# Kernel optimization log

Measured on AMD Instinct MI355X. Metric: run time of the kernel, lower is better.

Reference implementation:

```python
import math
import jax, jax.numpy as jnp
import numpy as np

B, L, D, H = 2, 2048, 1024, 16
HD = D // H  # head_size = 64


def setup_inputs() -> dict:
    key = jax.random.key(0)
    kx, kk, kq, kv, ko = jax.random.split(key, 5)
    scale = 1.0 / math.sqrt(D)
    return {
        "x": jax.random.normal(kx, (B, L, D), dtype=jnp.float32),
        "Wk": jax.random.normal(kk, (D, D), dtype=jnp.float32) * scale,
        "Wq": jax.random.normal(kq, (D, D), dtype=jnp.float32) * scale,
        "Wv": jax.random.normal(kv, (D, D), dtype=jnp.float32) * scale,
        "Wo": jax.random.normal(ko, (D, D), dtype=jnp.float32) * scale,
    }


def reference(x, Wk, Wq, Wv, Wo):
    # Projections (torch Linear without bias; weights pre-stored as [in, out])
    k = (x @ Wk).reshape(B, L, H, HD)
    q = (x @ Wq).reshape(B, L, H, HD)
    v = (x @ Wv).reshape(B, L, H, HD)
    # Per-head causal attention, vectorized over heads instead of python loop
    inv_sqrt_hd = 1.0 / math.sqrt(HD)
    scores = jnp.einsum("blhd,bmhd->bhlm", q, k) * inv_sqrt_hd  # [B,H,L,L]
    causal = jnp.tril(jnp.ones((L, L), dtype=bool))
    scores = jnp.where(causal, scores, -jnp.inf)
    probs = jax.nn.softmax(scores, axis=-1)
    # Dropout is identity in eval mode (reference baseline is deterministic)
    out = jnp.einsum("bhlm,bmhd->blhd", probs, v).reshape(B, L, D)
    return out @ Wo
```

## Files before the change

### kernel.cpp

```cpp
#include <hip/hip_runtime.h>
#include <cstdint>

#define B_ 2
#define L_ 2048
#define D_ 1024
#define H_ 16
#define HD_ 64
#define ML_ (B_ * L_)
#define S_ (3 * D_)
#define QK_LD 2048

typedef __bf16 bf16;
typedef __attribute__((ext_vector_type(4))) __bf16 bf16x4;
typedef __attribute__((ext_vector_type(8))) __bf16 bf16x8;
typedef __attribute__((ext_vector_type(4))) float f32x4;
typedef __attribute__((ext_vector_type(16))) float f32x16;

__device__ __forceinline__ f32x4 mfma_16x16x32(bf16x8 a, bf16x8 b, f32x4 c) {
    return __builtin_amdgcn_mfma_f32_16x16x32_bf16(a, b, c, 0, 0, 0);
}
__device__ __forceinline__ f32x16 mfma_32x32x16(bf16x8 a, bf16x8 b, f32x16 c) {
    return __builtin_amdgcn_mfma_f32_32x32x16_bf16(a, b, c, 0, 0, 0);
}

#define GLDS16(g, l)                                                              \
    __builtin_amdgcn_global_load_lds((const __attribute__((address_space(1))) void*)(g), \
                                     (__attribute__((address_space(3))) void*)(l), 16, 0, 0)

__global__ __launch_bounds__(256) void cast_x_kernel(const float* __restrict__ in,
                                                     bf16* __restrict__ out, int n4) {
    int i = blockIdx.x * blockDim.x + threadIdx.x;
    if (i >= n4) return;
    float4 v = reinterpret_cast<const float4*>(in)[i];
    bf16x4 o;
    o[0] = (bf16)v.x; o[1] = (bf16)v.y; o[2] = (bf16)v.z; o[3] = (bf16)v.w;
    reinterpret_cast<bf16x4*>(out)[i] = o;
}

__global__ __launch_bounds__(1024) void transpose_w_kernel(const float* __restrict__ W,
                                                           bf16* __restrict__ Wt) {
    __shared__ float tile[32][33];
    int n0 = blockIdx.x * 32, k0 = blockIdx.y * 32;
    int tx = threadIdx.x, ty = threadIdx.y;
    tile[ty][tx] = W[(size_t)(k0 + ty) * D_ + n0 + tx];
    __syncthreads();
    Wt[(size_t)(n0 + ty) * D_ + k0 + tx] = (bf16)tile[tx][ty];
}

template <typename OutT>
__global__ __launch_bounds__(256) void gemm128_kernel(const bf16* __restrict__ A,
                                                      const bf16* __restrict__ Bt,
                                                      OutT* __restrict__ C,
                                                      bf16* __restrict__ vt,
                                                      int M, int N, int K, int ldc) {
    __shared__ bf16 As[128][32];
    __shared__ bf16 Bs[128][32];
    const int nwg = gridDim.x;
    const int bid = (blockIdx.x & 7) * (nwg >> 3) + (blockIdx.x >> 3);
    const int nb = N >> 7;
    const int bm = bid / nb, bn = bid % nb;
    const int m0 = bm << 7, n0 = bn << 7;
    const int t = threadIdx.x;
    const int lane = t & 63;
    const int w = t >> 6;
    const int wm = w >> 1, wn = w & 1;
    const int fr = lane & 15, fk = (lane >> 4) << 3;
    const int srow = (w << 5) + (lane >> 2);
    const int scol = (lane & 3) << 3;

    f32x4 acc[4][4] = {};
    for (int k0 = 0; k0 < K; k0 += 32) {
        const bf16* ga0 = &A[(size_t)(m0 + srow) * K + k0 + scol];
        const bf16* ga1 = &A[(size_t)(m0 + srow + 16) * K + k0 + scol];
        const bf16* gb0 = &Bt[(size_t)(n0 + srow) * K + k0 + scol];
        const bf16* gb1 = &Bt[(size_t)(n0 + srow + 16) * K + k0 + scol];
        __syncthreads();
        GLDS16(ga0, &As[(w << 5)][0]);
        GLDS16(ga1, &As[(w << 5) + 16][0]);
        GLDS16(gb0, &Bs[(w << 5)][0]);
        GLDS16(gb1, &Bs[(w << 5) + 16][0]);
        __syncthreads();
        bf16x8 a[4], b[4];
#pragma unroll
        for (int mt = 0; mt < 4; ++mt)
            a[mt] = *reinterpret_cast<const bf16x8*>(&As[(wm << 6) + (mt << 4) + fr][fk]);
#pragma unroll
        for (int nt = 0; nt < 4; ++nt)
            b[nt] = *reinterpret_cast<const bf16x8*>(&Bs[(wn << 6) + (nt << 4) + fr][fk]);
#pragma unroll
        for (int mt = 0; mt < 4; ++mt)
#pragma unroll
            for (int nt = 0; nt < 4; ++nt)
                acc[mt][nt] = mfma_16x16x32(a[mt], b[nt], acc[mt][nt]);
    }
    const int col = lane & 15, rq = (lane >> 4) << 2;
    if (vt != nullptr && n0 >= 2048) {
#pragma unroll
        for (int mt = 0; mt < 4; ++mt)
#pragma unroll
            for (int nt = 0; nt < 4; ++nt) {
                int cc = n0 - 2048 + (wn << 6) + (nt << 4) + col;
                int rrb = m0 + (wm << 6) + (mt << 4) + rq;
                int bb = rrb >> 11, l = rrb & (L_ - 1);
                size_t vrow = ((size_t)bb * H_ + (cc >> 6)) * HD_ + (cc & 63);
                bf16x4 pk;
#pragma unroll
                for (int reg = 0; reg < 4; ++reg) pk[reg] = (bf16)acc[mt][nt][reg];
                *reinterpret_cast<bf16x4*>(&vt[vrow * L_ + l]) = pk;
            }
    } else {
#pragma unroll
        for (int mt = 0; mt < 4; ++mt)
#pragma unroll
            for (int nt = 0; nt < 4; ++nt)
#pragma unroll
                for (int reg = 0; reg < 4; ++reg) {
                    int rr = m0 + (wm << 6) + (mt << 4) + rq + reg;
                    int cc = n0 + (wn << 6) + (nt << 4) + col;
                    C[(size_t)rr * ldc + cc] = (OutT)acc[mt][nt][reg];
                }
    }
}

__global__ __launch_bounds__(256) void attn_kernel(const bf16* __restrict__ qk,
                                                   const bf16* __restrict__ vt,
                                                   bf16* __restrict__ O) {
    __shared__ bf16 Olds[4][32][72];
    const int nbh = B_ * H_;
    const int qt = (L_ / 128) - 1 - (int)(blockIdx.x / nbh);
    const int bh = blockIdx.x % nbh;
    const int h = bh % H_, b = bh / H_;
    const int t = threadIdx.x, lane = t & 63, w = t >> 6;
    const int li = lane & 31, hi = lane >> 5;
    const int qg0 = qt * 128 + w * 32;
    const int q_g = qg0 + li;

    const bf16* kbase = qk + (size_t)b * L_ * QK_LD + D_ + h * HD_;
    const bf16* vbase = vt + (size_t)bh * HD_ * L_;

    const bf16* qrow_p = qk + (size_t)(b * L_ + q_g) * QK_LD + h * HD_ + hi * 8;
    bf16x8 qB[4];
#pragma unroll
    for (int c = 0; c < 4; ++c) qB[c] = *reinterpret_cast<const bf16x8*>(qrow_p + c * 16);

    f32x16 ot0 = {}, ot1 = {};
    float mrun = -1e30f, lsum = 0.f;
    const float c1 = 0.18033688011112042f;

    const int nkb = (qg0 + 31) / 64 + 1;
    for (int kb = 0; kb < nkb; ++kb) {
        const int c0 = kb * 64;
        f32x16 st0 = {}, st1 = {};
        const bf16* kp0 = kbase + (size_t)(c0 + li) * QK_LD + hi * 8;
        const bf16* kp1 = kbase + (size_t)(c0 + 32 + li) * QK_LD + hi * 8;
#pragma unroll
        for (int c = 0; c < 4; ++c) {
            st0 = mfma_32x32x16(*reinterpret_cast<const bf16x8*>(kp0 + c * 16), qB[c], st0);
            st1 = mfma_32x32x16(*reinterpret_cast<const bf16x8*>(kp1 + c * 16), qB[c], st1);
        }
        float rm = -1e30f;
#pragma unroll
        for (int r = 0; r < 16; ++r) {
            const int kvl = (r & 3) + 8 * (r >> 2) + 4 * hi;
            float x0 = (c0 + kvl <= q_g) ? st0[r] * c1 : -1e30f;
            float x1 = (c0 + 32 + kvl <= q_g) ? st1[r] * c1 : -1e30f;
            st0[r] = x0; st1[r] = x1;
            rm = fmaxf(rm, fmaxf(x0, x1));
        }
        rm = fmaxf(rm, __shfl_xor(rm, 32));
        const float mn = fmaxf(mrun, rm);
        if (!__all(rm - mrun <= 8.0f)) {
            const float sc = exp2f(mrun - mn);
            lsum *= sc;
#pragma unroll
            for (int r = 0; r < 16; ++r) { ot0[r] *= sc; ot1[r] *= sc; }
            mrun = mn;
        }
        float rs = 0.f;
#pragma unroll
        for (int r = 0; r < 16; ++r) {
            float p0 = exp2f(st0[r] - mrun);
            float p1 = exp2f(st1[r] - mrun);
            st0[r] = p0; st1[r] = p1;
            rs += p0 + p1;
        }
        rs += __shfl_xor(rs, 32);
        lsum += rs;
        uint32_t wa[8], wb[8], ea[8], eb[8];
#pragma unroll
        for (int k = 0; k < 8; ++k) {
            asm("v_cvt_pk_bf16_f32 %0, %1, %2" : "=v"(wa[k]) : "v"(st0[2 * k]), "v"(st0[2 * k + 1]));
            asm("v_cvt_pk_bf16_f32 %0, %1, %2" : "=v"(wb[k]) : "v"(st1[2 * k]), "v"(st1[2 * k + 1]));
        }
#pragma unroll
        for (int k = 0; k < 8; ++k) {
            ea[k] = (uint32_t)__shfl_xor((int)wa[k], 32);
            eb[k] = (uint32_t)__shfl_xor((int)wb[k], 32);
        }
        union U8 { uint32_t u[4]; bf16x8 v; };
        U8 pb[4];
        pb[0].u[0] = hi ? ea[2] : wa[0]; pb[0].u[1] = hi ? ea[3] : wa[1];
        pb[0].u[2] = hi ? wa[2] : ea[0]; pb[0].u[3] = hi ? wa[3] : ea[1];
        pb[1].u[0] = hi ? ea[6] : wa[4]; pb[1].u[1] = hi ? ea[7] : wa[5];
        pb[1].u[2] = hi ? wa[6] : ea[4]; pb[1].u[3] = hi ? wa[7] : ea[5];
        pb[2].u[0] = hi ? eb[2] : wb[0]; pb[2].u[1] = hi ? eb[3] : wb[1];
        pb[2].u[2] = hi ? wb[2] : eb[0]; pb[2].u[3] = hi ? wb[3] : eb[1];
        pb[3].u[0] = hi ? eb[6] : wb[4]; pb[3].u[1] = hi ? eb[7] : wb[5];
        pb[3].u[2] = hi ? wb[6] : eb[4]; pb[3].u[3] = hi ? wb[7] : eb[5];
        const bf16* vp0 = vbase + (size_t)li * L_ + c0 + hi * 8;
        const bf16* vp1 = vbase + (size_t)(32 + li) * L_ + c0 + hi * 8;
#pragma unroll
        for (int j = 0; j < 4; ++j) {
            ot0 = mfma_32x32x16(*reinterpret_cast<const bf16x8*>(vp0 + j * 16), pb[j].v, ot0);
            ot1 = mfma_32x32x16(*reinterpret_cast<const bf16x8*>(vp1 + j * 16), pb[j].v, ot1);
        }
    }
    const float rinv = 1.0f / lsum;
#pragma unroll
    for (int r2 = 0; r2 < 8; ++r2) {
        const int hd0 = 2 * (r2 & 1) + 8 * (r2 >> 1) + 4 * hi;
        uint32_t u0, u1;
        float a0 = ot0[2 * r2] * rinv, a1 = ot0[2 * r2 + 1] * rinv;
        float b0 = ot1[2 * r2] * rinv, b1 = ot1[2 * r2 + 1] * rinv;
        asm("v_cvt_pk_bf16_f32 %0, %1, %2" : "=v"(u0) : "v"(a0), "v"(a1));
        asm("v_cvt_pk_bf16_f32 %0, %1, %2" : "=v"(u1) : "v"(b0), "v"(b1));
        *reinterpret_cast<uint32_t*>(&Olds[w][li][hd0]) = u0;
        *reinterpret_cast<uint32_t*>(&Olds[w][li][32 + hd0]) = u1;
    }
    __syncthreads();
    const int qr = lane >> 1, half = lane & 1;
    const size_t orow = ((size_t)b * L_ + qt * 128 + w * 32 + qr) * D_ + h * HD_ + half * 32;
#pragma unroll
    for (int k = 0; k < 4; ++k) {
        bf16x8 vv = *reinterpret_cast<const bf16x8*>(&Olds[w][qr][half * 32 + k * 8]);
        *reinterpret_cast<bf16x8*>(&O[orow + k * 8]) = vv;
    }
}

extern "C" void kernel_launch(void* const* d_in, const int* in_sizes, int n_in,
                              void* d_out, int out_size, void* d_ws, size_t ws_size,
                              hipStream_t stream) {
    const float* x = (const float*)d_in[0];
    const float* Wk = (const float*)d_in[1];
    const float* Wq = (const float*)d_in[2];
    const float* Wv = (const float*)d_in[3];
    const float* Wo = (const float*)d_in[4];
    float* out = (float*)d_out;

    char* p = (char*)d_ws;
    const size_t xsz = (size_t)ML_ * D_ * sizeof(bf16);
    const size_t wsz = (size_t)D_ * D_ * sizeof(bf16);
    bf16* xb = (bf16*)p;   p += xsz;
    bf16* Wc = (bf16*)p;   p += 3 * wsz;
    bf16* Wot = (bf16*)p;  p += wsz;
    bf16* qkb = (bf16*)p;  p += (size_t)ML_ * QK_LD * sizeof(bf16);
    bf16* vtb = (bf16*)p;  p += xsz;
    bf16* ab = xb;

    const int n4 = ML_ * D_ / 4;
    cast_x_kernel<<<(n4 + 255) / 256, 256, 0, stream>>>(x, xb, n4);
    dim3 tb(32, 32);
    dim3 tg(D_ / 32, D_ / 32);
    transpose_w_kernel<<<tg, tb, 0, stream>>>(Wq, Wc);
    transpose_w_kernel<<<tg, tb, 0, stream>>>(Wk, Wc + (size_t)D_ * D_);
    transpose_w_kernel<<<tg, tb, 0, stream>>>(Wv, Wc + 2 * (size_t)D_ * D_);
    transpose_w_kernel<<<tg, tb, 0, stream>>>(Wo, Wot);

    gemm128_kernel<bf16><<<(ML_ / 128) * (S_ / 128), 256, 0, stream>>>(
        xb, Wc, qkb, vtb, ML_, S_, D_, QK_LD);

    attn_kernel<<<B_ * H_ * (L_ / 128), 256, 0, stream>>>(qkb, vtb, ab);

    gemm128_kernel<float><<<(ML_ / 128) * (D_ / 128), 256, 0, stream>>>(
        ab, Wot, out, nullptr, ML_, D_, D_, D_);
}
```

Baseline: 253.3 us.

## Split attention KV loop across paired waves and merge partial softmax states

Attention blocks now use 512 threads, with two waves per 32-row query group. Each wave processes alternating 64-key blocks, and the two partial (max, sum, output) states are merged through shared memory at the end. This doubles the waves working on each query group to shorten the serial causal loop. The change also interleaves the query-tile order so long and short tiles mix, skips masking on fully unmasked key blocks, and uses tree reductions for the row max and row sum. The cost is more LDS, an extra sync and merge step, and possibly lower occupancy from the larger blocks.

```diff
diff --git a/kernel.cpp b/kernel.cpp
--- a/kernel.cpp
+++ b/kernel.cpp
@@ -122,17 +122,20 @@
     }
 }
 
-__global__ __launch_bounds__(256) void attn_kernel(const bf16* __restrict__ qk,
-                                                   const bf16* __restrict__ vt,
-                                                   bf16* __restrict__ O) {
+__global__ __launch_bounds__(512, 4) void attn_kernel(const bf16* __restrict__ qk,
+                                                      const bf16* __restrict__ vt,
+                                                      bf16* __restrict__ O) {
+    __shared__ float Mrg[4][34][64];
     __shared__ bf16 Olds[4][32][72];
     const int nbh = B_ * H_;
-    const int qt = (L_ / 128) - 1 - (int)(blockIdx.x / nbh);
+    const int g = (int)(blockIdx.x / nbh);
+    const int qt = (g < 8) ? (15 - g) : (g - 8);
     const int bh = blockIdx.x % nbh;
     const int h = bh % H_, b = bh / H_;
     const int t = threadIdx.x, lane = t & 63, w = t >> 6;
+    const int p = w >> 1, s = w & 1;
     const int li = lane & 31, hi = lane >> 5;
-    const int qg0 = qt * 128 + w * 32;
+    const int qg0 = qt * 128 + p * 32;
     const int q_g = qg0 + li;
 
     const bf16* kbase = qk + (size_t)b * L_ * QK_LD + D_ + h * HD_;
@@ -148,26 +151,35 @@
     const float c1 = 0.18033688011112042f;
 
     const int nkb = (qg0 + 31) / 64 + 1;
-    for (int kb = 0; kb < nkb; ++kb) {
+    for (int kb = s; kb < nkb; kb += 2) {
         const int c0 = kb * 64;
         f32x16 st0 = {}, st1 = {};
         const bf16* kp0 = kbase + (size_t)(c0 + li) * QK_LD + hi * 8;
-        const bf16* kp1 = kbase + (size_t)(c0 + 32 + li) * QK_LD + hi * 8;
+        const bf16* kp1 = kp0 + (size_t)32 * QK_LD;
 #pragma unroll
         for (int c = 0; c < 4; ++c) {
             st0 = mfma_32x32x16(*reinterpret_cast<const bf16x8*>(kp0 + c * 16), qB[c], st0);
             st1 = mfma_32x32x16(*reinterpret_cast<const bf16x8*>(kp1 + c * 16), qB[c], st1);
         }
-        float rm = -1e30f;
-#pragma unroll
-        for (int r = 0; r < 16; ++r) {
-            const int kvl = (r & 3) + 8 * (r >> 2) + 4 * hi;
-            float x0 = (c0 + kvl <= q_g) ? st0[r] * c1 : -1e30f;
-            float x1 = (c0 + 32 + kvl <= q_g) ? st1[r] * c1 : -1e30f;
-            st0[r] = x0; st1[r] = x1;
-            rm = fmaxf(rm, fmaxf(x0, x1));
-        }
-        rm = fmaxf(rm, __shfl_xor(rm, 32));
+        if (c0 + 64 <= qg0) {
+#pragma unroll
+            for (int r = 0; r < 16; ++r) { st0[r] *= c1; st1[r] *= c1; }
+        } else {
+#pragma unroll
+            for (int r = 0; r < 16; ++r) {
+                const int kvl = (r & 3) + 8 * (r >> 2) + 4 * hi;
+                st0[r] = (c0 + kvl <= q_g) ? st0[r] * c1 : -1e30f;
+                st1[r] = (c0 + 32 + kvl <= q_g) ? st1[r] * c1 : -1e30f;
+            }
+        }
+        float mx[16];
+#pragma unroll
+        for (int r = 0; r < 16; ++r) mx[r] = fmaxf(st0[r], st1[r]);
+#pragma unroll
+        for (int d = 8; d > 0; d >>= 1)
+#pragma unroll
+            for (int r = 0; r < d; ++r) mx[r] = fmaxf(mx[r], mx[r + d]);
+        const float rm = fmaxf(mx[0], __shfl_xor(mx[0], 32));
         const float mn = fmaxf(mrun, rm);
         if (!__all(rm - mrun <= 8.0f)) {
             const float sc = exp2f(mrun - mn);
@@ -176,16 +188,19 @@
             for (int r = 0; r < 16; ++r) { ot0[r] *= sc; ot1[r] *= sc; }
             mrun = mn;
         }
-        float rs = 0.f;
+        float sm[16];
 #pragma unroll
         for (int r = 0; r < 16; ++r) {
             float p0 = exp2f(st0[r] - mrun);
             float p1 = exp2f(st1[r] - mrun);
             st0[r] = p0; st1[r] = p1;
-            rs += p0 + p1;
-        }
-        rs += __shfl_xor(rs, 32);
-        lsum += rs;
+            sm[r] = p0 + p1;
+        }
+#pragma unroll
+        for (int d = 8; d > 0; d >>= 1)
+#pragma unroll
+            for (int r = 0; r < d; ++r) sm[r] += sm[r + d];
+        lsum += sm[0] + __shfl_xor(sm[0], 32);
         uint32_t wa[8], wb[8], ea[8], eb[8];
 #pragma unroll
         for (int k = 0; k < 8; ++k) {
@@ -215,25 +230,46 @@
             ot1 = mfma_32x32x16(*reinterpret_cast<const bf16x8*>(vp1 + j * 16), pb[j].v, ot1);
         }
     }
-    const float rinv = 1.0f / lsum;
-#pragma unroll
-    for (int r2 = 0; r2 < 8; ++r2) {
-        const int hd0 = 2 * (r2 & 1) + 8 * (r2 >> 1) + 4 * hi;
-        uint32_t u0, u1;
-        float a0 = ot0[2 * r2] * rinv, a1 = ot0[2 * r2 + 1] * rinv;
-        float b0 = ot1[2 * r2] * rinv, b1 = ot1[2 * r2 + 1] * rinv;
-        asm("v_cvt_pk_bf16_f32 %0, %1, %2" : "=v"(u0) : "v"(a0), "v"(a1));
-        asm("v_cvt_pk_bf16_f32 %0, %1, %2" : "=v"(u1) : "v"(b0), "v"(b1));
-        *reinterpret_cast<uint32_t*>(&Olds[w][li][hd0]) = u0;
-        *reinterpret_cast<uint32_t*>(&Olds[w][li][32 + hd0]) = u1;
+    if (s == 1) {
+#pragma unroll
+        for (int r = 0; r < 16; ++r) {
+            Mrg[p][r][lane] = ot0[r];
+            Mrg[p][16 + r][lane] = ot1[r];
+        }
+        Mrg[p][32][lane] = mrun;
+        Mrg[p][33][lane] = lsum;
     }
     __syncthreads();
-    const int qr = lane >> 1, half = lane & 1;
-    const size_t orow = ((size_t)b * L_ + qt * 128 + w * 32 + qr) * D_ + h * HD_ + half * 32;
-#pragma unroll
-    for (int k = 0; k < 4; ++k) {
-        bf16x8 vv = *reinterpret_cast<const bf16x8*>(&Olds[w][qr][half * 32 + k * 8]);
-        *reinterpret_cast<bf16x8*>(&O[orow + k * 8]) = vv;
+    if (s == 0) {
+        const float m1 = Mrg[p][32][lane], l1 = Mrg[p][33][lane];
+        const float M = fmaxf(mrun, m1);
+        const float sc0 = exp2f(mrun - M), sc1 = exp2f(m1 - M);
+        const float rinv = 1.0f / (lsum * sc0 + l1 * sc1);
+        const float f0 = sc0 * rinv, f1 = sc1 * rinv;
+#pragma unroll
+        for (int r2 = 0; r2 < 8; ++r2) {
+            const int hd0 = 2 * (r2 & 1) + 8 * (r2 >> 1) + 4 * hi;
+            uint32_t u0, u1;
+            float a0 = ot0[2 * r2] * f0 + Mrg[p][2 * r2][lane] * f1;
+            float a1 = ot0[2 * r2 + 1] * f0 + Mrg[p][2 * r2 + 1][lane] * f1;
+            float b0 = ot1[2 * r2] * f0 + Mrg[p][16 + 2 * r2][lane] * f1;
+            float b1 = ot1[2 * r2 + 1] * f0 + Mrg[p][16 + 2 * r2 + 1][lane] * f1;
+            asm("v_cvt_pk_bf16_f32 %0, %1, %2" : "=v"(u0) : "v"(a0), "v"(a1));
+            asm("v_cvt_pk_bf16_f32 %0, %1, %2" : "=v"(u1) : "v"(b0), "v"(b1));
+            *reinterpret_cast<uint32_t*>(&Olds[p][li][hd0]) = u0;
+            *reinterpret_cast<uint32_t*>(&Olds[p][li][32 + hd0]) = u1;
+        }
+    }
+    __syncthreads();
+    if (s == 0) {
+        const int qr = lane >> 1, half = lane & 1;
+        const size_t orow =
+            ((size_t)b * L_ + qt * 128 + p * 32 + qr) * D_ + h * HD_ + half * 32;
+#pragma unroll
+        for (int k = 0; k < 4; ++k) {
+            bf16x8 vv = *reinterpret_cast<const bf16x8*>(&Olds[p][qr][half * 32 + k * 8]);
+            *reinterpret_cast<bf16x8*>(&O[orow + k * 8]) = vv;
+        }
     }
 }
 
@@ -269,7 +305,7 @@
     gemm128_kernel<bf16><<<(ML_ / 128) * (S_ / 128), 256, 0, stream>>>(
         xb, Wc, qkb, vtb, ML_, S_, D_, QK_LD);
 
-    attn_kernel<<<B_ * H_ * (L_ / 128), 256, 0, stream>>>(qkb, vtb, ab);
+    attn_kernel<<<B_ * H_ * (L_ / 128), 512, 0, stream>>>(qkb, vtb, ab);
 
     gemm128_kernel<float><<<(ML_ / 128) * (D_ / 128), 256, 0, stream>>>(
         ab, Wot, out, nullptr, ML_, D_, D_, D_);
```

Result: slower. 316.3 us (+24.9%).
